# Kernel optimization log

Measured on AMD Instinct MI355X. Metric: run time of the kernel, lower is better.

The kernel has to match this reference:

```python
import jax, jax.numpy as jnp
import numpy as np

NUM_HEADS = 12


def get_rel_pos(q_size, k_size, rel_pos):
    # rel_pos: (2*max(q,k)-1, C). Here q_size==k_size so no interpolation needed.
    q_coords = jnp.arange(q_size)[:, None] * max(k_size / q_size, 1.0)
    k_coords = jnp.arange(k_size)[None, :] * max(q_size / k_size, 1.0)
    rel = (q_coords - k_coords) + (k_size - 1) * max(q_size / k_size, 1.0)
    return rel_pos[rel.astype(jnp.int32)]  # (q_size, k_size, C)


def add_decomposed_rel_pos(attn, q, rel_pos_h, rel_pos_w, q_size, k_size):
    q_h, q_w = q_size
    k_h, k_w = k_size
    Rh = get_rel_pos(q_h, k_h, rel_pos_h)  # (q_h,k_h,C)
    Rw = get_rel_pos(q_w, k_w, rel_pos_w)  # (q_w,k_w,C)
    B, _, C = q.shape  # B = num_heads * batch
    r_q = q.reshape(B, q_h, q_w, C)
    rel_h = jnp.einsum('bhwc,hkc->bhwk', r_q, Rh)  # (B,q_h,q_w,k_h)
    rel_w = jnp.einsum('bhwc,wkc->bhwk', r_q, Rw)  # (B,q_h,q_w,k_w)
    attn = attn.reshape(B, q_h, q_w, k_h, k_w)
    attn = attn + rel_h[:, :, :, :, None] + rel_w[:, :, :, None, :]
    return attn.reshape(B, q_h * q_w, k_h * k_w)


def setup_inputs() -> dict:
    key = jax.random.key(0)
    ks = jax.random.split(key, 7)
    B, H, W, dim = 128, 14, 14, 768
    head_dim = dim // NUM_HEADS
    return {
        'x': jax.random.normal(ks[0], (B, H, W, dim), dtype=jnp.float32),
        'qkv_w': jax.random.normal(ks[1], (dim, 3 * dim), dtype=jnp.float32) * 0.02,
        'qkv_b': jax.random.normal(ks[2], (3 * dim,), dtype=jnp.float32) * 0.02,
        'proj_w': jax.random.normal(ks[3], (dim, dim), dtype=jnp.float32) * 0.02,
        'proj_b': jax.random.normal(ks[4], (dim,), dtype=jnp.float32) * 0.02,
        'rel_pos_h': jax.random.normal(ks[5], (2 * H - 1, head_dim), dtype=jnp.float32) * 0.02,
        'rel_pos_w': jax.random.normal(ks[6], (2 * W - 1, head_dim), dtype=jnp.float32) * 0.02,
    }


def reference(x, qkv_w, qkv_b, proj_w, proj_b, rel_pos_h, rel_pos_w):
    B, H, W, dim = x.shape
    nh = NUM_HEADS
    hd = dim // nh
    scale = hd ** -0.5
    L = H * W
    # qkv projection: (B,H,W,3*dim) -> (3, nh*B, L, hd)
    qkv = x.reshape(B, L, dim) @ qkv_w + qkv_b
    qkv = qkv.reshape(B, L, 3, nh, hd)
    qkv = jnp.transpose(qkv, (2, 3, 0, 1, 4)).reshape(3, nh * B, L, hd)
    q, k, v = qkv[0], qkv[1], qkv[2]
    attn = jnp.einsum('bqc,bkc->bqk', q * scale, k)  # (nh*B, L, L)
    attn = add_decomposed_rel_pos(attn, q, rel_pos_h, rel_pos_w, (H, W), (H, W))
    attn = jax.nn.softmax(attn, axis=-1)
    out = jnp.einsum('bqk,bkc->bqc', attn, v)  # (nh*B, L, hd)
    out = out.reshape(nh, B, H, W, hd)
    out = jnp.transpose(out, (1, 2, 3, 0, 4)).reshape(B, H, W, dim)
    return out @ proj_w + proj_b
```

## Files before the change

kernel.cpp:

```cpp
#include <hip/hip_runtime.h>
#include <stdint.h>
#include <math.h>

typedef unsigned short u16;
typedef __bf16 bf16x8 __attribute__((ext_vector_type(8)));
typedef u16 u16x8 __attribute__((ext_vector_type(8)));
typedef float f32x4 __attribute__((ext_vector_type(4)));

#define MFMA16(a,b,c) __builtin_amdgcn_mfma_f32_16x16x32_bf16((a),(b),(c),0,0,0)
#define GLOAD16(gp, lp) __builtin_amdgcn_global_load_lds( \
    (const __attribute__((address_space(1))) void*)(gp), \
    (__attribute__((address_space(3))) void*)(lp), 16, 0, 0)

__device__ __forceinline__ u16 f2bf(float f) {
  union { float f; uint32_t u; } v; v.f = f;
  return (u16)((v.u + 0x7FFFu + ((v.u >> 16) & 1u)) >> 16);
}
__device__ __forceinline__ float bits2f(uint32_t u) {
  union { uint32_t u; float f; } v; v.u = u; return v.f;
}
__device__ __forceinline__ uint32_t cvtpk(float lo, float hi) {
  uint32_t r;
  asm("v_cvt_pk_bf16_f32 %0, %1, %2" : "=v"(r) : "v"(lo), "v"(hi));
  return r;
}
__device__ __forceinline__ int4 pack8(const u16* v) {
  int4 r;
  r.x = (int)((uint32_t)v[0] | ((uint32_t)v[1] << 16));
  r.y = (int)((uint32_t)v[2] | ((uint32_t)v[3] << 16));
  r.z = (int)((uint32_t)v[4] | ((uint32_t)v[5] << 16));
  r.w = (int)((uint32_t)v[6] | ((uint32_t)v[7] << 16));
  return r;
}

__global__ void k_cvt(const float* __restrict__ in, u16* __restrict__ out, int n4, float scale) {
  int i = blockIdx.x * 256 + threadIdx.x;
  int stride = gridDim.x * 256;
  for (; i < n4; i += stride) {
    float4 v = reinterpret_cast<const float4*>(in)[i];
    ushort4 o;
    o.x = f2bf(v.x * scale); o.y = f2bf(v.y * scale);
    o.z = f2bf(v.z * scale); o.w = f2bf(v.w * scale);
    reinterpret_cast<ushort4*>(out)[i] = o;
  }
}

__global__ void k_transpose(const float* __restrict__ in, u16* __restrict__ out, int R, int C) {
  __shared__ float t[32][33];
  int tx = threadIdx.x & 31, ty = threadIdx.x >> 5;
  int c0 = blockIdx.x * 32, r0 = blockIdx.y * 32;
  #pragma unroll
  for (int i = 0; i < 4; i++)
    t[ty + i*8][tx] = in[(size_t)(r0 + ty + i*8) * C + (c0 + tx)];
  __syncthreads();
  #pragma unroll
  for (int i = 0; i < 4; i++)
    out[(size_t)(c0 + ty + i*8) * R + (r0 + tx)] = f2bf(t[tx][ty + i*8]);
}

__global__ __launch_bounds__(512, 2) void k_qkv256(
    const u16* __restrict__ A, const u16* __restrict__ BT, const float* __restrict__ bias,
    u16* __restrict__ qo, u16* __restrict__ ko, u16* __restrict__ vo)
{
  __shared__ u16 SMEM[65536];

  int bid0 = blockIdx.x;
  int xcd = bid0 & 7, idx = bid0 >> 3;
  int base = (xcd < 2) ? xcd * 111 : 2 * 111 + (xcd - 2) * 110;
  int wgid = base + idx;
  int mt = wgid / 9, nt = wgid - (wgid / 9) * 9;

  int tid = threadIdx.x, lane = tid & 63, w = tid >> 6;
  int g = lane >> 4, c4 = lane & 15;
  int wr = w >> 2, wc = w & 3;

  int srow = lane >> 2;
  int pslot = (lane & 3) ^ ((lane >> 3) & 3);
  int cidA = w * 2;

  const u16* pA1 = A + (size_t)(mt * 256 + cidA * 16 + srow) * 768 + pslot * 8;
  const u16* pA2 = pA1 + 16 * 768;
  const u16* pB1 = BT + (size_t)(nt * 256 + cidA * 16 + srow) * 768 + pslot * 8;
  const u16* pB2 = pB1 + 16 * 768;

  int rsel = g ^ ((c4 >> 1) & 3);
  int aoff = wr * 4096 + c4 * 32 + rsel * 8;
  int boff = wc * 2048 + c4 * 32 + rsel * 8;

  f32x4 acc[8][4];
  f32x4 z4 = {0.f, 0.f, 0.f, 0.f};
  #pragma unroll
  for (int f = 0; f < 8; f++)
    #pragma unroll
    for (int fc = 0; fc < 4; fc++) acc[f][fc] = z4;

  #pragma unroll
  for (int kk = 0; kk < 3; kk++) {
    u16* dA = SMEM + kk * 8192;
    GLOAD16(pA1 + kk * 32, dA + cidA * 512);
    GLOAD16(pA2 + kk * 32, dA + (cidA + 1) * 512);
    u16* dB = SMEM + 32768 + kk * 8192;
    GLOAD16(pB1 + kk * 32, dB + cidA * 512);
    GLOAD16(pB2 + kk * 32, dB + (cidA + 1) * 512);
  }
  asm volatile("s_waitcnt vmcnt(8)" ::: "memory");
  __builtin_amdgcn_s_barrier();

  for (int k = 0; k < 24; ++k) {
    const u16* As = SMEM + (k & 3) * 8192;
    const u16* Bs = SMEM + 32768 + (k & 3) * 8192;
    bf16x8 bfr[4], afr[4];
    #pragma unroll
    for (int fc = 0; fc < 4; fc++) bfr[fc] = *(const bf16x8*)(Bs + boff + fc * 512);
    #pragma unroll
    for (int f = 0; f < 4; f++) afr[f] = *(const bf16x8*)(As + aoff + f * 512);
    if (k < 21) {
      u16* d = SMEM + ((k + 3) & 3) * 8192;
      GLOAD16(pA1 + (k + 3) * 32, d + cidA * 512);
      GLOAD16(pA2 + (k + 3) * 32, d + (cidA + 1) * 512);
      asm volatile("s_waitcnt vmcnt(6)" ::: "memory");
    } else if (k == 21) {
      asm volatile("s_waitcnt vmcnt(0)" ::: "memory");
    }
    __builtin_amdgcn_s_barrier();
    __builtin_amdgcn_s_setprio(1);
    #pragma unroll
    for (int f = 0; f < 4; f++)
      #pragma unroll
      for (int fc = 0; fc < 4; fc++)
        acc[f][fc] = MFMA16(afr[f], bfr[fc], acc[f][fc]);
    __builtin_amdgcn_s_setprio(0);

    #pragma unroll
    for (int f = 0; f < 4; f++) afr[f] = *(const bf16x8*)(As + aoff + (4 + f) * 512);
    if (k < 21) {
      u16* d = SMEM + 32768 + ((k + 3) & 3) * 8192;
      GLOAD16(pB1 + (k + 3) * 32, d + cidA * 512);
      GLOAD16(pB2 + (k + 3) * 32, d + (cidA + 1) * 512);
      asm volatile("s_waitcnt vmcnt(6)" ::: "memory");
    }
    __builtin_amdgcn_s_barrier();
    __builtin_amdgcn_s_setprio(1);
    #pragma unroll
    for (int f = 0; f < 4; f++)
      #pragma unroll
      for (int fc = 0; fc < 4; fc++)
        acc[4 + f][fc] = MFMA16(afr[f], bfr[fc], acc[4 + f][fc]);
    __builtin_amdgcn_s_setprio(0);
  }

  int i3 = nt / 3;
  u16* dst = (i3 == 0) ? qo : (i3 == 1) ? ko : vo;
  int head = (nt - i3 * 3) * 4 + wc;
  float bsv[4];
  #pragma unroll
  for (int fc = 0; fc < 4; fc++) bsv[fc] = bias[nt * 256 + wc * 64 + fc * 16 + c4];

  int mbase = mt * 256 + wr * 128 + g * 4;
  #pragma unroll
  for (int f = 0; f < 8; f++) {
    #pragma unroll
    for (int j = 0; j < 4; j++) {
      int mm = mbase + f * 16 + j;
      int bb2 = mm / 196, ll = mm - bb2 * 196;
      size_t ro = (size_t)((head * 128 + bb2) * 196 + ll) * 64;
      #pragma unroll
      for (int fc = 0; fc < 4; fc++)
        dst[ro + fc * 16 + c4] = f2bf(acc[f][fc][j] + bsv[fc]);
    }
  }
}

__device__ __forceinline__ void rd_frags8(const u16* As_, const u16* Bs_, int aoff, int boff,
                                          bf16x8 (&b)[4], bf16x8 (&a)[4]) {
  #pragma unroll
  for (int fc = 0; fc < 4; fc++) b[fc] = *(const bf16x8*)(Bs_ + boff + fc * 512);
  #pragma unroll
  for (int f = 0; f < 4; f++) a[f] = *(const bf16x8*)(As_ + aoff + f * 512);
}

__global__ __launch_bounds__(256, 2) void k_proj256(
    const u16* __restrict__ A, const u16* __restrict__ BT, const float* __restrict__ bias,
    float* __restrict__ out)
{
  __shared__ u16 SMEM[32768];

  int bid0 = blockIdx.x;
  int bid = (bid0 & 7) * 147 + (bid0 >> 3);
  int nt = bid % 6, mt = bid / 6;

  int tid = threadIdx.x, lane = tid & 63, w = tid >> 6;
  int g = lane >> 4, c4 = lane & 15;
  int wr = w >> 1, wc = w & 1;

  int srow = lane >> 2;
  int pslot = (lane & 3) ^ ((lane >> 3) & 3);
  int cidA = w * 2;

  const u16* pA1 = A + (size_t)(mt * 128 + cidA * 16 + srow) * 768 + pslot * 8;
  const u16* pA2 = pA1 + 16 * 768;
  const u16* pB1 = BT + (size_t)(nt * 128 + cidA * 16 + srow) * 768 + pslot * 8;
  const u16* pB2 = pB1 + 16 * 768;

  int rsel = g ^ ((c4 >> 1) & 3);
  int aoff = wr * 2048 + c4 * 32 + rsel * 8;
  int boff = wc * 2048 + c4 * 32 + rsel * 8;

  f32x4 acc[4][4];
  f32x4 z4 = {0.f, 0.f, 0.f, 0.f};
  #pragma unroll
  for (int f = 0; f < 4; f++)
    #pragma unroll
    for (int fc = 0; fc < 4; fc++) acc[f][fc] = z4;

  #pragma unroll
  for (int kk = 0; kk < 3; kk++) {
    u16* dA = SMEM + kk * 4096;
    GLOAD16(pA1 + kk * 32, dA + cidA * 512);
    GLOAD16(pA2 + kk * 32, dA + (cidA + 1) * 512);
    u16* dB = SMEM + 16384 + kk * 4096;
    GLOAD16(pB1 + kk * 32, dB + cidA * 512);
    GLOAD16(pB2 + kk * 32, dB + (cidA + 1) * 512);
  }
  asm volatile("s_waitcnt vmcnt(8)" ::: "memory");
  __builtin_amdgcn_s_barrier();

  for (int k = 0; k < 24; ++k) {
    const u16* As = SMEM + (k & 3) * 4096;
    const u16* Bs = SMEM + 16384 + (k & 3) * 4096;
    bf16x8 bfr[4], afr[4];
    rd_frags8(As, Bs, aoff, boff, bfr, afr);
    if (k < 21) {
      u16* dA = SMEM + ((k + 3) & 3) * 4096;
      GLOAD16(pA1 + (k + 3) * 32, dA + cidA * 512);
      GLOAD16(pA2 + (k + 3) * 32, dA + (cidA + 1) * 512);
      u16* dB = SMEM + 16384 + ((k + 3) & 3) * 4096;
      GLOAD16(pB1 + (k + 3) * 32, dB + cidA * 512);
      GLOAD16(pB2 + (k + 3) * 32, dB + (cidA + 1) * 512);
      asm volatile("s_waitcnt vmcnt(8)" ::: "memory");
    } else if (k == 21) {
      asm volatile("s_waitcnt vmcnt(4)" ::: "memory");
    } else if (k == 22) {
      asm volatile("s_waitcnt vmcnt(0)" ::: "memory");
    }
    __builtin_amdgcn_s_barrier();
    __builtin_amdgcn_s_setprio(1);
    #pragma unroll
    for (int f = 0; f < 4; f++)
      #pragma unroll
      for (int fc = 0; fc < 4; fc++)
        acc[f][fc] = MFMA16(afr[f], bfr[fc], acc[f][fc]);
    __builtin_amdgcn_s_setprio(0);
    __builtin_amdgcn_s_barrier();
  }

  #pragma unroll
  for (int fc = 0; fc < 4; fc++) {
    int n0 = nt * 128 + wc * 64 + fc * 16 + c4;
    float bs = bias[n0];
    #pragma unroll
    for (int fr = 0; fr < 4; fr++)
      #pragma unroll
      for (int j = 0; j < 4; j++) {
        int m = mt * 128 + wr * 64 + fr * 16 + g * 4 + j;
        out[(size_t)m * 768 + n0] = acc[fr][fc][j] + bs;
      }
  }
}

#define VP 232
__global__ __launch_bounds__(256, 2) void k_attn(
    const u16* __restrict__ Q, const u16* __restrict__ Kg, const u16* __restrict__ Vg,
    const u16* __restrict__ RPH, const u16* __restrict__ RPW, u16* __restrict__ Ows)
{
  __shared__ u16 K64[208 * 64];
  __shared__ u16 Krel[208 * 40];
  __shared__ u16 VT[64 * VP];
  __shared__ u16 Qrel[4][16 * 40];

  int bh = blockIdx.x;
  int hh = bh >> 7, bb = bh & 127;
  int tid = threadIdx.x, lane = tid & 63, w = tid >> 6;
  int g = lane >> 4, c4 = lane & 15;

  const u16* kbase = Kg + (size_t)bh * 12544;
  const u16* vbase = Vg + (size_t)bh * 12544;
  const u16* qbase = Q + (size_t)bh * 12544;

  const float KSC = 0.18033688011f;
  for (int ch = tid; ch < 1664; ch += 256) {
    int row = ch >> 3, s = ch & 7;
    u16 outv[8];
    if (row < 196) {
      u16x8 v = *(const u16x8*)(kbase + row * 64 + s * 8);
      #pragma unroll
      for (int e = 0; e < 8; e++)
        outv[e] = f2bf(bits2f((uint32_t)v[e] << 16) * KSC);
    } else {
      #pragma unroll
      for (int e = 0; e < 8; e++) outv[e] = 0;
    }
    *(int4*)(K64 + row * 64 + ((s ^ (row & 7)) * 8)) = pack8(outv);
  }
  if (tid < 208) {
    int k = tid;
    int kh = k / 14, kw2 = k - kh * 14;
    #pragma unroll
    for (int s = 0; s < 5; s++) {
      u16 vals[8];
      #pragma unroll
      for (int e = 0; e < 8; e++) {
        int c = s * 8 + e;
        u16 x = 0;
        if (k < 196) {
          if (c == kh) x = 0x3F80;
          else if (c == 14 + kw2) x = 0x3F80;
        } else {
          if (c == 28) x = 0x3F80;
        }
        vals[e] = x;
      }
      *(int4*)(Krel + k * 40 + s * 8) = pack8(vals);
    }
  }
  for (int i = tid; i < 2048; i += 256) {
    int chn = i >> 5, c = 192 + (i & 31);
    if (c >= 196 && c < VP) VT[chn * VP + c] = 0;
  }
  for (int ch2 = tid; ch2 < 784; ch2 += 256) {
    int kp = ch2 % 98, cb = ch2 / 98;
    int key = kp * 2, cz = cb * 8;
    u16x8 a = *(const u16x8*)(vbase + key * 64 + cz);
    u16x8 b2 = *(const u16x8*)(vbase + (key + 1) * 64 + cz);
    int kk = key & 31;
    int colp = (key >> 5) * 32 + ((kk & 15) >> 2) * 8 + (kk & 3) + ((kk >> 4) << 2);
    #pragma unroll
    for (int j = 0; j < 8; j++) {
      uint32_t pk = (uint32_t)a[j] | ((uint32_t)b2[j] << 16);
      *(uint32_t*)(VT + (cz + j) * VP + colp) = pk;
    }
  }
  __syncthreads();

  int t1 = 16 + c4; if (t1 > 26) t1 = 26;
  bf16x8 rh00 = *(const bf16x8*)(RPH + c4 * 64 + g * 8);
  bf16x8 rh01 = *(const bf16x8*)(RPH + c4 * 64 + 32 + g * 8);
  bf16x8 rh10 = *(const bf16x8*)(RPH + t1 * 64 + g * 8);
  bf16x8 rh11 = *(const bf16x8*)(RPH + t1 * 64 + 32 + g * 8);
  bf16x8 rw00 = *(const bf16x8*)(RPW + c4 * 64 + g * 8);
  bf16x8 rw01 = *(const bf16x8*)(RPW + c4 * 64 + 32 + g * 8);
  bf16x8 rw10 = *(const bf16x8*)(RPW + t1 * 64 + g * 8);
  bf16x8 rw11 = *(const bf16x8*)(RPW + t1 * 64 + 32 + g * 8);

  f32x4 z4 = {0.f, 0.f, 0.f, 0.f};

  int qi0 = w * 16 + c4;
  int qr0 = qi0 > 195 ? 195 : qi0;
  bf16x8 qa0 = *(const bf16x8*)(qbase + qr0 * 64 + g * 8);
  bf16x8 qa1 = *(const bf16x8*)(qbase + qr0 * 64 + 32 + g * 8);

  for (int qt = w; qt < 13; qt += 4) {
    int qi = qt * 16 + c4;
    bf16x8 nq0, nq1;
    int qn = qt + 4;
    if (qn < 13) {
      int qrn = qn * 16 + c4; if (qrn > 195) qrn = 195;
      nq0 = *(const bf16x8*)(qbase + qrn * 64 + g * 8);
      nq1 = *(const bf16x8*)(qbase + qrn * 64 + 32 + g * 8);
    }

    u16* Qr = (u16*)Qrel[w];
    {
      int4 zz = {0, 0, 0, 0};
      *(int4*)(Qr + lane * 8) = zz;
      if (lane < 16) *(int4*)(Qr + 512 + lane * 8) = zz;
      if (g == 0) Qr[c4 * 40 + 28] = f2bf(-30000.f);
    }

    int qh = qi / 14;
    int qwv = qi - qh * 14;

    f32x4 e0 = MFMA16(rh00, qa0, z4); e0 = MFMA16(rh01, qa1, e0);
    f32x4 e1 = MFMA16(rh10, qa0, z4); e1 = MFMA16(rh11, qa1, e1);
    #pragma unroll
    for (int tt = 0; tt < 2; tt++) {
      f32x4 e = tt ? e1 : e0;
      #pragma unroll
      for (int j = 0; j < 4; j++) {
        int t = tt * 16 + 4 * g + j;
        int kh = qh + 13 - t;
        if ((unsigned)kh <= 13u) Qr[c4 * 40 + kh] = f2bf(e[j]);
      }
    }
    f32x4 f0 = MFMA16(rw00, qa0, z4); f0 = MFMA16(rw01, qa1, f0);
    f32x4 f1 = MFMA16(rw10, qa0, z4); f1 = MFMA16(rw11, qa1, f1);
    #pragma unroll
    for (int tt = 0; tt < 2; tt++) {
      f32x4 e = tt ? f1 : f0;
      #pragma unroll
      for (int j = 0; j < 4; j++) {
        int t = tt * 16 + 4 * g + j;
        int kw3 = qwv + 13 - t;
        if ((unsigned)kw3 <= 13u) Qr[c4 * 40 + 14 + kw3] = f2bf(e[j]);
      }
    }

    bf16x8 qrelB = *(const bf16x8*)(Qr + c4 * 40 + g * 8);

    f32x4 St[13];
    #pragma unroll
    for (int i = 0; i < 13; i++) {
      int key = i * 16 + c4;
      const u16* kr = K64 + key * 64;
      int sw = key & 7;
      bf16x8 kb0 = *(const bf16x8*)(kr + ((g ^ sw) * 8));
      bf16x8 kb1 = *(const bf16x8*)(kr + (((4 + g) ^ sw) * 8));
      f32x4 acc = MFMA16(kb0, qa0, z4);
      acc = MFMA16(kb1, qa1, acc);
      bf16x8 krl = *(const bf16x8*)(Krel + key * 40 + g * 8);
      St[i] = MFMA16(krl, qrelB, acc);
    }

    float mx = -3.0e38f;
    #pragma unroll
    for (int i = 0; i < 13; i++)
      #pragma unroll
      for (int j = 0; j < 4; j++) mx = fmaxf(mx, St[i][j]);
    mx = fmaxf(mx, __shfl_xor(mx, 16));
    mx = fmaxf(mx, __shfl_xor(mx, 32));

    float ls = 0.f;
    f32x4 O[4] = {z4, z4, z4, z4};
    #pragma unroll
    for (int p = 0; p < 7; p++) {
      float pe[8];
      #pragma unroll
      for (int j2 = 0; j2 < 4; j2++) { pe[j2] = exp2f(St[2 * p][j2] - mx); ls += pe[j2]; }
      if (p < 6) {
        #pragma unroll
        for (int j2 = 0; j2 < 4; j2++) { pe[4 + j2] = exp2f(St[2 * p + 1][j2] - mx); ls += pe[4 + j2]; }
      } else {
        #pragma unroll
        for (int j2 = 0; j2 < 4; j2++) pe[4 + j2] = 0.f;
      }
      union { uint32_t u[4]; bf16x8 v; } pb;
      pb.u[0] = cvtpk(pe[0], pe[1]);
      pb.u[1] = cvtpk(pe[2], pe[3]);
      pb.u[2] = cvtpk(pe[4], pe[5]);
      pb.u[3] = cvtpk(pe[6], pe[7]);
      #pragma unroll
      for (int ct = 0; ct < 4; ct++) {
        bf16x8 va = *(const bf16x8*)(VT + (ct * 16 + c4) * VP + p * 32 + g * 8);
        O[ct] = MFMA16(va, pb.v, O[ct]);
      }
    }
    ls += __shfl_xor(ls, 16);
    ls += __shfl_xor(ls, 32);

    if (qi < 196) {
      float inv = 1.f / ls;
      size_t obase = (size_t)(bb * 196 + qi) * 768 + hh * 64;
      #pragma unroll
      for (int ct = 0; ct < 4; ct++) {
        uint32_t o0 = cvtpk(O[ct][0] * inv, O[ct][1] * inv);
        uint32_t o1 = cvtpk(O[ct][2] * inv, O[ct][3] * inv);
        uint2 ov = {o0, o1};
        *(uint2*)(Ows + obase + ct * 16 + g * 4) = ov;
      }
    }
    qa0 = nq0; qa1 = nq1;
  }
}

extern "C" void kernel_launch(void* const* d_in, const int* in_sizes, int n_in,
                              void* d_out, int out_size, void* d_ws, size_t ws_size,
                              hipStream_t stream) {
  (void)in_sizes; (void)n_in; (void)out_size; (void)ws_size;
  const float* x      = (const float*)d_in[0];
  const float* qkv_w  = (const float*)d_in[1];
  const float* qkv_b  = (const float*)d_in[2];
  const float* proj_w = (const float*)d_in[3];
  const float* proj_b = (const float*)d_in[4];
  const float* rph    = (const float*)d_in[5];
  const float* rpw    = (const float*)d_in[6];
  float* out = (float*)d_out;
  char* ws = (char*)d_ws;

  u16* xb   = (u16*)(ws);
  u16* wT   = (u16*)(ws + 38535168);
  u16* pT   = (u16*)(ws + 42074112);
  u16* rphb = (u16*)(ws + 43253760);
  u16* rpwb = (u16*)(ws + 43257856);
  u16* qws  = (u16*)(ws + 43261952);
  u16* kws  = (u16*)(ws + 81797120);
  u16* vws  = (u16*)(ws + 120332288);
  u16* Ows  = xb;

  const float LOG2E = 1.44269504f;
  k_cvt<<<2048, 256, 0, stream>>>(x, xb, 4816896, 1.0f);
  k_cvt<<<2, 256, 0, stream>>>(rph, rphb, 432, LOG2E);
  k_cvt<<<2, 256, 0, stream>>>(rpw, rpwb, 432, LOG2E);
  k_transpose<<<dim3(72, 24), 256, 0, stream>>>(qkv_w, wT, 768, 2304);
  k_transpose<<<dim3(24, 24), 256, 0, stream>>>(proj_w, pT, 768, 768);
  k_qkv256<<<882, 512, 0, stream>>>(xb, wT, qkv_b, qws, kws, vws);
  k_attn<<<1536, 256, 0, stream>>>(qws, kws, vws, rphb, rpwb, Ows);
  k_proj256<<<1176, 256, 0, stream>>>(Ows, pT, proj_b, out);
}
```

Measured before the change: 272.0 us.

## Restructure QKV GEMM mainloop to BK=64 double-buffered tiles with split fragment loads

The QKV projection GEMM mainloop moves from a 4-stage ring of BK=32 tiles to a 2-stage double buffer of BK=64 tiles, with a new XOR swizzle for 128-byte rows and a new global-to-LDS staging layout. Each iteration now loads both k-halves of the fragments up front and issues the first half's MFMAs after a partial lgkmcnt wait. It then syncs once and prefetches the tile two steps ahead before the second half's MFMAs. The aim is to halve the barrier count per unit of K and overlap LDS reads with MFMA issue. The cost is more fragment registers and shallower prefetch depth, which could hurt latency hiding.

```diff
diff --git a/kernel.cpp b/kernel.cpp
--- a/kernel.cpp
+++ b/kernel.cpp
@@ -11,6 +11,7 @@
 #define GLOAD16(gp, lp) __builtin_amdgcn_global_load_lds( \
     (const __attribute__((address_space(1))) void*)(gp), \
     (__attribute__((address_space(3))) void*)(lp), 16, 0, 0)
+#define BARRIER_FENCED() asm volatile("s_barrier" ::: "memory")
 
 __device__ __forceinline__ u16 f2bf(float f) {
   union { float f; uint32_t u; } v; v.f = f;
@@ -74,18 +75,21 @@
   int g = lane >> 4, c4 = lane & 15;
   int wr = w >> 2, wc = w & 3;
 
-  int srow = lane >> 2;
-  int pslot = (lane & 3) ^ ((lane >> 3) & 3);
-  int cidA = w * 2;
-
-  const u16* pA1 = A + (size_t)(mt * 256 + cidA * 16 + srow) * 768 + pslot * 8;
-  const u16* pA2 = pA1 + 16 * 768;
-  const u16* pB1 = BT + (size_t)(nt * 256 + cidA * 16 + srow) * 768 + pslot * 8;
-  const u16* pB2 = pB1 + 16 * 768;
-
-  int rsel = g ^ ((c4 >> 1) & 3);
-  int aoff = wr * 4096 + c4 * 32 + rsel * 8;
-  int boff = wc * 2048 + c4 * 32 + rsel * 8;
+  int strow = tid >> 3;
+  int sslot = (tid & 7) ^ ((tid >> 3) & 7);
+  const u16* pA[4];
+  const u16* pB[4];
+  #pragma unroll
+  for (int c = 0; c < 4; c++) {
+    pA[c] = A + (size_t)(mt * 256 + c * 64 + strow) * 768 + sslot * 8;
+    pB[c] = BT + (size_t)(nt * 256 + c * 64 + strow) * 768 + sslot * 8;
+  }
+  int ldsw = w * 512;
+
+  int rs0 = (g ^ (c4 & 7)) * 8;
+  int rs1 = ((4 + g) ^ (c4 & 7)) * 8;
+  int abase = wr * 8192 + c4 * 64;
+  int bbase = 32768 + (wc >> 1) * 8192 + ((wc & 1) * 64 + c4) * 64;
 
   f32x4 acc[8][4];
   f32x4 z4 = {0.f, 0.f, 0.f, 0.f};
@@ -94,60 +98,64 @@
     #pragma unroll
     for (int fc = 0; fc < 4; fc++) acc[f][fc] = z4;
 
-  #pragma unroll
-  for (int kk = 0; kk < 3; kk++) {
-    u16* dA = SMEM + kk * 8192;
-    GLOAD16(pA1 + kk * 32, dA + cidA * 512);
-    GLOAD16(pA2 + kk * 32, dA + (cidA + 1) * 512);
-    u16* dB = SMEM + 32768 + kk * 8192;
-    GLOAD16(pB1 + kk * 32, dB + cidA * 512);
-    GLOAD16(pB2 + kk * 32, dB + (cidA + 1) * 512);
-  }
+#define STAGE_QKV(KT)                                                        \
+  {                                                                          \
+    u16* ab_ = SMEM + ((KT) & 1) * 16384 + ldsw;                             \
+    u16* bb_ = SMEM + 32768 + ((KT) & 1) * 16384 + ldsw;                     \
+    _Pragma("unroll") for (int c_ = 0; c_ < 4; c_++)                         \
+      GLOAD16(pA[c_] + (KT) * 64, ab_ + c_ * 4096);                          \
+    _Pragma("unroll") for (int c_ = 0; c_ < 4; c_++)                         \
+      GLOAD16(pB[c_] + (KT) * 64, bb_ + c_ * 4096);                          \
+  }
+
+  STAGE_QKV(0)
+  STAGE_QKV(1)
   asm volatile("s_waitcnt vmcnt(8)" ::: "memory");
-  __builtin_amdgcn_s_barrier();
-
-  for (int k = 0; k < 24; ++k) {
-    const u16* As = SMEM + (k & 3) * 8192;
-    const u16* Bs = SMEM + 32768 + (k & 3) * 8192;
-    bf16x8 bfr[4], afr[4];
-    #pragma unroll
-    for (int fc = 0; fc < 4; fc++) bfr[fc] = *(const bf16x8*)(Bs + boff + fc * 512);
-    #pragma unroll
-    for (int f = 0; f < 4; f++) afr[f] = *(const bf16x8*)(As + aoff + f * 512);
-    if (k < 21) {
-      u16* d = SMEM + ((k + 3) & 3) * 8192;
-      GLOAD16(pA1 + (k + 3) * 32, d + cidA * 512);
-      GLOAD16(pA2 + (k + 3) * 32, d + (cidA + 1) * 512);
-      asm volatile("s_waitcnt vmcnt(6)" ::: "memory");
-    } else if (k == 21) {
-      asm volatile("s_waitcnt vmcnt(0)" ::: "memory");
-    }
-    __builtin_amdgcn_s_barrier();
+  BARRIER_FENCED();
+
+  for (int kt = 0; kt < 12; ++kt) {
+    const u16* Td = SMEM + (kt & 1) * 16384;
+    bf16x8 a0[8], b0[4], a1[8], b1[4];
+    #pragma unroll
+    for (int f = 0; f < 8; f++) a0[f] = *(const bf16x8*)(Td + abase + f * 1024 + rs0);
+    #pragma unroll
+    for (int n = 0; n < 4; n++) b0[n] = *(const bf16x8*)(Td + bbase + n * 1024 + rs0);
+    __builtin_amdgcn_sched_barrier(0);
+    #pragma unroll
+    for (int f = 0; f < 8; f++) a1[f] = *(const bf16x8*)(Td + abase + f * 1024 + rs1);
+    #pragma unroll
+    for (int n = 0; n < 4; n++) b1[n] = *(const bf16x8*)(Td + bbase + n * 1024 + rs1);
+
+    asm volatile("s_waitcnt lgkmcnt(12)" ::: "memory");
+    __builtin_amdgcn_sched_barrier(0);
     __builtin_amdgcn_s_setprio(1);
     #pragma unroll
-    for (int f = 0; f < 4; f++)
+    for (int f = 0; f < 8; f++)
       #pragma unroll
       for (int fc = 0; fc < 4; fc++)
-        acc[f][fc] = MFMA16(afr[f], bfr[fc], acc[f][fc]);
+        acc[f][fc] = MFMA16(a0[f], b0[fc], acc[f][fc]);
     __builtin_amdgcn_s_setprio(0);
 
-    #pragma unroll
-    for (int f = 0; f < 4; f++) afr[f] = *(const bf16x8*)(As + aoff + (4 + f) * 512);
-    if (k < 21) {
-      u16* d = SMEM + 32768 + ((k + 3) & 3) * 8192;
-      GLOAD16(pB1 + (k + 3) * 32, d + cidA * 512);
-      GLOAD16(pB2 + (k + 3) * 32, d + (cidA + 1) * 512);
-      asm volatile("s_waitcnt vmcnt(6)" ::: "memory");
-    }
-    __builtin_amdgcn_s_barrier();
+    asm volatile("s_waitcnt lgkmcnt(0)" ::: "memory");
+    __builtin_amdgcn_sched_barrier(0);
+    BARRIER_FENCED();
+
+    if (kt < 10) STAGE_QKV(kt + 2)
+
     __builtin_amdgcn_s_setprio(1);
     #pragma unroll
-    for (int f = 0; f < 4; f++)
+    for (int f = 0; f < 8; f++)
       #pragma unroll
       for (int fc = 0; fc < 4; fc++)
-        acc[4 + f][fc] = MFMA16(afr[f], bfr[fc], acc[4 + f][fc]);
+        acc[f][fc] = MFMA16(a1[f], b1[fc], acc[f][fc]);
     __builtin_amdgcn_s_setprio(0);
-  }
+
+    if (kt < 10)       { asm volatile("s_waitcnt vmcnt(8)" ::: "memory"); }
+    else if (kt == 10) { asm volatile("s_waitcnt vmcnt(0)" ::: "memory"); }
+    __builtin_amdgcn_sched_barrier(0);
+    BARRIER_FENCED();
+  }
+#undef STAGE_QKV
 
   int i3 = nt / 3;
   u16* dst = (i3 == 0) ? qo : (i3 == 1) ? ko : vo;
```

Result: no change. 273.0 us (+0.4%).
